# Optimization experiments

Hardware: AMD Instinct MI355X
Metric: run time of the kernel (lower is better)

## Reference

```python
import jax, jax.numpy as jnp
import numpy as np

H = 8  # head_num

def setup_inputs() -> dict:
    key = jax.random.key(0)
    k1, k2, k3, k4, k5 = jax.random.split(key, 5)
    n, e = 4096, 128
    x = jax.random.normal(k1, (n, e), dtype=jnp.float32)
    # torch Linear weights stored here as [in, out]; scale ~ 1/sqrt(fan_in)
    w_qkv = jax.random.normal(k2, (e, e * 3 * H), dtype=jnp.float32) * (1.0 / np.sqrt(e))
    b_qkv = jax.random.normal(k3, (e * 3 * H,), dtype=jnp.float32) * 0.01
    w_proj = jax.random.normal(k4, (e * H, e), dtype=jnp.float32) * (1.0 / np.sqrt(e * H))
    b_proj = jax.random.normal(k5, (e,), dtype=jnp.float32) * 0.01
    return {"x": x, "w_qkv": w_qkv, "b_qkv": b_qkv, "w_proj": w_proj, "b_proj": b_proj}

def reference(x, w_qkv, b_qkv, w_proj, b_proj):
    n, e = x.shape
    # packed layout along output dim is (h, d, qkv) per rearrange 'n (h d qkv) -> qkv h n d'
    qkv = (x @ w_qkv + b_qkv).reshape(n, H, e, 3)          # [n, h, d, 3]
    q = jnp.transpose(qkv[..., 0], (1, 0, 2))              # [h, n, d]
    k = jnp.transpose(qkv[..., 1], (1, 0, 2))
    v = jnp.transpose(qkv[..., 2], (1, 0, 2))
    energy = jnp.einsum('hqd,hkd->hqk', q, k)              # [h, n, n]
    scaling = jnp.asarray(e, x.dtype) ** 0.5
    att = jax.nn.softmax(energy, axis=-1) / scaling        # post-softmax scale (as in source)
    out = jnp.einsum('hqk,hkd->hqd', att, v)               # [h, n, d]
    out = jnp.transpose(out, (1, 0, 2)).reshape(n, H * e)  # [n, h*d]
    return out @ w_proj + b_proj
```

## Files before the change

kernel.cpp:

```cpp
#include <hip/hip_runtime.h>
#include <hip/hip_fp16.h>


#define N_TOK 4096
#define DH 128
#define NH 8

#define EXP2F(x) __builtin_amdgcn_exp2f(x)

typedef _Float16 f16;
typedef __attribute__((ext_vector_type(8))) _Float16 f16x8;
typedef __attribute__((ext_vector_type(2))) __fp16 hf2;
typedef __attribute__((ext_vector_type(4))) float f32x4;

#define GLD16(gsrc, ldst) __builtin_amdgcn_global_load_lds( \
    (const __attribute__((address_space(1))) void*)(gsrc), \
    (__attribute__((address_space(3))) void*)(ldst), 16, 0, 0)

__global__ __launch_bounds__(256) void conv_wproj(
    const float* __restrict__ w_proj, f16* __restrict__ wpT)
{
  int t = blockIdx.x * 256 + threadIdx.x;
  int k = t >> 7, col = t & 127;
  wpT[col * 1024 + k] = (f16)w_proj[t];
}

__global__ __launch_bounds__(256) void conv_wqkv(
    const float* __restrict__ w_qkv, const float* __restrict__ b_qkv,
    f16* __restrict__ wqkvT, float* __restrict__ bperm)
{
  int t = blockIdx.x * 256 + threadIdx.x;
  int k = t / 3072;
  int col = t - k * 3072;
  int hh = col / 384;
  int rem = col - hh * 384;
  int d = rem / 3;
  int s = rem - d * 3;
  int colp = s * 1024 + hh * 128 + d;
  float scale = (s == 0) ? 1.4426950408889634f : 1.0f;
  wqkvT[colp * 128 + k] = (f16)(w_qkv[t] * scale);
  if (k == 0) bperm[colp] = b_qkv[col] * scale;
}

__global__ __launch_bounds__(256) void qkv_gemm2(
    const float* __restrict__ x, const f16* __restrict__ wqkvT,
    const float* __restrict__ bperm,
    f16* __restrict__ Qh, f16* __restrict__ Kh, f16* __restrict__ Vt)
{
  const int cb = blockIdx.x;
  const int rb = blockIdx.y;
  const int tid = threadIdx.x;
  const int w = tid >> 6, lane = tid & 63;
  const int l16 = lane & 15, lhi = lane >> 4;
  const int s = cb >> 3, h = cb & 7;

  f16x8 xf[2][4];
#pragma unroll
  for (int m = 0; m < 2; ++m)
#pragma unroll
    for (int kt = 0; kt < 4; ++kt) {
      const float* xp = x + (size_t)(rb * 128 + w * 32 + m * 16 + l16) * 128 + kt * 32 + lhi * 8;
      f32x4 x0 = *(const f32x4*)xp, x1 = *(const f32x4*)(xp + 4);
      f16x8 v;
#pragma unroll
      for (int j = 0; j < 4; ++j) { v[j] = (f16)x0[j]; v[4 + j] = (f16)x1[j]; }
      xf[m][kt] = v;
    }

  f32x4 acc[8][2];
#pragma unroll
  for (int nt = 0; nt < 8; ++nt)
#pragma unroll
    for (int m = 0; m < 2; ++m) acc[nt][m] = (f32x4){0.f, 0.f, 0.f, 0.f};

#pragma unroll
  for (int nt = 0; nt < 8; ++nt)
#pragma unroll
    for (int kt = 0; kt < 4; ++kt) {
      f16x8 wf = *(const f16x8*)(wqkvT + (size_t)(cb * 128 + nt * 16 + l16) * 128 + kt * 32 + lhi * 8);
      acc[nt][0] = __builtin_amdgcn_mfma_f32_16x16x32_f16(wf, xf[0][kt], acc[nt][0], 0, 0, 0);
      acc[nt][1] = __builtin_amdgcn_mfma_f32_16x16x32_f16(wf, xf[1][kt], acc[nt][1], 0, 0, 0);
    }

#pragma unroll
  for (int nt = 0; nt < 8; ++nt) {
    f32x4 bb = *(const f32x4*)(bperm + cb * 128 + nt * 16 + 4 * lhi);
#pragma unroll
    for (int m = 0; m < 2; ++m) acc[nt][m] += bb;
  }

  if (s == 2) {
#pragma unroll
    for (int nt = 0; nt < 8; ++nt)
#pragma unroll
      for (int m = 0; m < 2; ++m)
#pragma unroll
        for (int r = 0; r < 4; ++r)
          Vt[(size_t)(h * 128 + nt * 16 + 4 * lhi + r) * N_TOK + rb * 128 + w * 32 + m * 16 + l16] =
              (f16)acc[nt][m][r];
  } else {
    __shared__ f16 tr[128][136];
#pragma unroll
    for (int nt = 0; nt < 8; ++nt)
#pragma unroll
      for (int m = 0; m < 2; ++m)
#pragma unroll
        for (int r = 0; r < 4; ++r)
          tr[w * 32 + m * 16 + l16][nt * 16 + 4 * lhi + r] = (f16)acc[nt][m][r];
    __syncthreads();
    f16* dst = (s == 0 ? Qh : Kh) + (size_t)(h * N_TOK + rb * 128) * 128;
    int r = tid >> 1, dh = (tid & 1) * 64;
#pragma unroll
    for (int i = 0; i < 8; ++i)
      *(f16x8*)(dst + r * 128 + dh + i * 8) = *(const f16x8*)(&tr[r][dh + i * 8]);
  }
}

__global__ __launch_bounds__(512, 2) void flash_attn(
    const f16* __restrict__ Qh, const f16* __restrict__ Kh,
    const f16* __restrict__ Vt, f16* __restrict__ opart, float* __restrict__ mlpart)
{
  const int bid = blockIdx.x;
  const int h = bid & 7, sp = (bid >> 3) & 1, qb = bid >> 4;
  const int tid = threadIdx.x;
  const int w = tid >> 6, lane = tid & 63;
  const int l16 = lane & 15, lhi = lane >> 4;

  __shared__ __align__(16) char smem[65536];

  f16x8 qf[2][4];
#pragma unroll
  for (int m = 0; m < 2; ++m)
#pragma unroll
    for (int kt = 0; kt < 4; ++kt)
      qf[m][kt] = *(const f16x8*)(Qh +
          (size_t)(h * N_TOK + qb * 256 + w * 32 + m * 16 + l16) * DH + kt * 32 + lhi * 8);

  int koff[4][4], voff[2][8];
#pragma unroll
  for (int nt = 0; nt < 4; ++nt) {
    int row = 32 * (nt >> 1) + 8 * (l16 >> 2) + 4 * (nt & 1) + (l16 & 3);
    int fk = (row & 3) | ((row & 8) >> 1);
#pragma unroll
    for (int kt = 0; kt < 4; ++kt)
      koff[nt][kt] = row * 256 + ((kt * 4 + lhi) ^ fk) * 16;
  }
#pragma unroll
  for (int ks = 0; ks < 2; ++ks)
#pragma unroll
    for (int dt = 0; dt < 8; ++dt) {
      int rowv = dt * 16 + l16;
      voff[ks][dt] = rowv * 128 + (((ks * 4 + lhi) ^ (rowv & 7))) * 16;
    }

  f32x4 o[2][8];
#pragma unroll
  for (int m = 0; m < 2; ++m)
#pragma unroll
    for (int dt = 0; dt < 8; ++dt) o[m][dt] = (f32x4){0.f, 0.f, 0.f, 0.f};
  float mrun[2] = {-3e38f, -3e38f}, lrun[2] = {0.f, 0.f};

  const f16* Kgh = Kh + (size_t)h * N_TOK * DH;
  const f16* Vgh = Vt + (size_t)h * DH * N_TOK;

  auto stage = [&](int buf, int kb) {
    char* kd = smem + buf * 16384;
    char* vd = smem + 32768 + buf * 16384;
#pragma unroll
    for (int c2 = 0; c2 < 2; ++c2) {
      int c = w * 2 + c2;
      {
        int row = c * 4 + (lane >> 4);
        int fk = (row & 3) | ((row & 8) >> 1);
        const f16* src = Kgh + (size_t)(kb * 64 + row) * DH + ((lane & 15) ^ fk) * 8;
        GLD16(src, kd + c * 1024);
      }
      {
        int row = c * 8 + (lane >> 3);
        const f16* src = Vgh + (size_t)row * N_TOK + kb * 64 + ((lane & 7) ^ (row & 7)) * 8;
        GLD16(src, vd + c * 1024);
      }
    }
  };

  const int kb0 = sp * 32;
  stage(0, kb0);
  __syncthreads();
  int buf = 0;
  for (int kb = kb0; kb < kb0 + 32; ++kb) {
    if (kb < kb0 + 31) stage(buf ^ 1, kb + 1);
    const char* kd = smem + buf * 16384;
    const char* vd = smem + 32768 + buf * 16384;

    f32x4 sv[2][4];
    __builtin_amdgcn_s_setprio(1);
#pragma unroll
    for (int nt = 0; nt < 4; ++nt) {
      f32x4 a0 = {0.f, 0.f, 0.f, 0.f}, a1 = {0.f, 0.f, 0.f, 0.f};
#pragma unroll
      for (int kt = 0; kt < 4; ++kt) {
        f16x8 kf = *(const f16x8*)(kd + koff[nt][kt]);
        a0 = __builtin_amdgcn_mfma_f32_16x16x32_f16(kf, qf[0][kt], a0, 0, 0, 0);
        a1 = __builtin_amdgcn_mfma_f32_16x16x32_f16(kf, qf[1][kt], a1, 0, 0, 0);
      }
      sv[0][nt] = a0; sv[1][nt] = a1;
    }
    __builtin_amdgcn_s_setprio(0);

    f16x8 pf[2][2];
#pragma unroll
    for (int m = 0; m < 2; ++m) {
      f32x4 mv;
#pragma unroll
      for (int r = 0; r < 4; ++r)
        mv[r] = fmaxf(fmaxf(sv[m][0][r], sv[m][1][r]), fmaxf(sv[m][2][r], sv[m][3][r]));
      float pmax = fmaxf(fmaxf(mv[0], mv[1]), fmaxf(mv[2], mv[3]));
      if (!__all(pmax - mrun[m] <= 8.f)) {
        float rm = fmaxf(pmax, __shfl_xor(pmax, 16));
        rm = fmaxf(rm, __shfl_xor(rm, 32));
        float mnew = fmaxf(mrun[m], rm);
        float sc = EXP2F(mrun[m] - mnew);
        lrun[m] *= sc;
#pragma unroll
        for (int dt = 0; dt < 8; ++dt) o[m][dt] *= sc;
        mrun[m] = mnew;
      }
      float mr = mrun[m];
      f32x4 ps = {0.f, 0.f, 0.f, 0.f};
#pragma unroll
      for (int nt = 0; nt < 4; ++nt)
#pragma unroll
        for (int r = 0; r < 4; ++r) {
          float p = EXP2F(sv[m][nt][r] - mr);
          sv[m][nt][r] = p;
          ps[r] += p;
        }
      lrun[m] += (ps[0] + ps[1]) + (ps[2] + ps[3]);
#pragma unroll
      for (int ks = 0; ks < 2; ++ks) {
        union { f16x8 v; hf2 hh[4]; } u;
        u.hh[0] = __builtin_amdgcn_cvt_pkrtz(sv[m][2 * ks][0], sv[m][2 * ks][1]);
        u.hh[1] = __builtin_amdgcn_cvt_pkrtz(sv[m][2 * ks][2], sv[m][2 * ks][3]);
        u.hh[2] = __builtin_amdgcn_cvt_pkrtz(sv[m][2 * ks + 1][0], sv[m][2 * ks + 1][1]);
        u.hh[3] = __builtin_amdgcn_cvt_pkrtz(sv[m][2 * ks + 1][2], sv[m][2 * ks + 1][3]);
        pf[m][ks] = u.v;
      }
    }

    __builtin_amdgcn_s_setprio(1);
#pragma unroll
    for (int ks = 0; ks < 2; ++ks)
#pragma unroll
      for (int dt = 0; dt < 8; ++dt) {
        f16x8 vf = *(const f16x8*)(vd + voff[ks][dt]);
        o[0][dt] = __builtin_amdgcn_mfma_f32_16x16x32_f16(vf, pf[0][ks], o[0][dt], 0, 0, 0);
        o[1][dt] = __builtin_amdgcn_mfma_f32_16x16x32_f16(vf, pf[1][ks], o[1][dt], 0, 0, 0);
      }
    __builtin_amdgcn_s_setprio(0);

    __syncthreads();
    buf ^= 1;
  }

  f16* ob = opart + ((size_t)((sp * 8 + h) * 16 + qb)) * 32768;
  float* mlb = mlpart + ((size_t)((sp * 8 + h) * 16 + qb)) * 512;
#pragma unroll
  for (int m = 0; m < 2; ++m) {
    float lr = lrun[m];
    lr += __shfl_xor(lr, 16);
    lr += __shfl_xor(lr, 32);
    float rl = 1.0f / lr;
#pragma unroll
    for (int dt = 0; dt < 8; ++dt)
#pragma unroll
      for (int r = 0; r < 4; ++r)
        ob[(dt * 16 + 4 * lhi + r) * 256 + w * 32 + m * 16 + l16] = (f16)(o[m][dt][r] * rl);
    if (lhi == 0) {
      mlb[w * 32 + m * 16 + l16] = mrun[m];
      mlb[256 + w * 32 + m * 16 + l16] = lr;
    }
  }
}

__global__ __launch_bounds__(256) void proj_combine(
    const f16* __restrict__ opart, const float* __restrict__ mlpart,
    const f16* __restrict__ wpT, const float* __restrict__ b_proj,
    float* __restrict__ out)
{
  const int tid = threadIdx.x;
  const int w = tid >> 6;
  const int lane = tid & 63;
  const int l16 = lane & 15, lhi = lane >> 4;
  const int rb = blockIdx.x * 16;
  const int qb = rb >> 8;
  const int nl0 = rb & 255;

  __shared__ f16 A[16][1032];
  __shared__ float wl[8][16][3];
  __shared__ float red[4][16][128];

  const float isc = 0.08838834764831845f;
  if (tid < 128) {
    int hh = tid >> 4, n = tid & 15;
    const float* ml0 = mlpart + ((size_t)((0 + hh) * 16 + qb)) * 512 + nl0 + n;
    const float* ml1 = mlpart + ((size_t)((8 + hh) * 16 + qb)) * 512 + nl0 + n;
    float m0 = ml0[0], l0 = ml0[256], m1 = ml1[0], l1 = ml1[256];
    float mt = fmaxf(m0, m1);
    float n0 = EXP2F(m0 - mt) * l0, n1 = EXP2F(m1 - mt) * l1;
    wl[hh][n][0] = n0; wl[hh][n][1] = n1;
    wl[hh][n][2] = isc / (n0 + n1);
  }
  __syncthreads();

  {
    int d = tid >> 1, nn = (tid & 1) * 8;
#pragma unroll
    for (int hh = 0; hh < 8; ++hh) {
      const f16* O0 = opart + ((size_t)((0 + hh) * 16 + qb)) * 32768 + d * 256 + nl0 + nn;
      const f16* O1 = opart + ((size_t)((8 + hh) * 16 + qb)) * 32768 + d * 256 + nl0 + nn;
      f16x8 a0 = *(const f16x8*)O0, a1 = *(const f16x8*)O1;
#pragma unroll
      for (int j = 0; j < 8; ++j) {
        int n = nn + j;
        float v = ((float)a0[j] * wl[hh][n][0] + (float)a1[j] * wl[hh][n][1]) * wl[hh][n][2];
        A[n][hh * 128 + d] = (f16)v;
      }
    }
  }
  __syncthreads();

  f32x4 o[8];
#pragma unroll
  for (int dt = 0; dt < 8; ++dt) o[dt] = (f32x4){0.f, 0.f, 0.f, 0.f};

#pragma unroll
  for (int kb = 0; kb < 8; ++kb) {
    int k0 = w * 256 + kb * 32 + lhi * 8;
    f16x8 a = *(const f16x8*)(&A[l16][k0]);
#pragma unroll
    for (int dt = 0; dt < 8; ++dt) {
      f16x8 b = *(const f16x8*)(wpT + (size_t)(dt * 16 + l16) * 1024 + k0);
      o[dt] = __builtin_amdgcn_mfma_f32_16x16x32_f16(a, b, o[dt], 0, 0, 0);
    }
  }

#pragma unroll
  for (int dt = 0; dt < 8; ++dt)
#pragma unroll
    for (int r = 0; r < 4; ++r)
      red[w][lhi * 4 + r][dt * 16 + l16] = o[dt][r];
  __syncthreads();
#pragma unroll
  for (int i = 0; i < 8; ++i) {
    int idx = tid + 256 * i;
    int row = idx >> 7, col = idx & 127;
    float v = red[0][row][col] + red[1][row][col] + red[2][row][col]
            + red[3][row][col] + b_proj[col];
    out[(size_t)(rb + row) * 128 + col] = v;
  }
}

extern "C" void kernel_launch(void* const* d_in, const int* in_sizes, int n_in,
                              void* d_out, int out_size, void* d_ws, size_t ws_size,
                              hipStream_t stream) {
  const float* x      = (const float*)d_in[0];
  const float* w_qkv  = (const float*)d_in[1];
  const float* b_qkv  = (const float*)d_in[2];
  const float* w_proj = (const float*)d_in[3];
  const float* b_proj = (const float*)d_in[4];
  float* out = (float*)d_out;

  char* ws = (char*)d_ws;
  const size_t MB = 1024 * 1024;
  f16*   Qh     = (f16*)(ws);
  f16*   Kh     = (f16*)(ws + 8 * MB);
  f16*   Vt     = (f16*)(ws + 16 * MB);
  f16*   opart  = (f16*)(ws + 24 * MB);
  float* mlpart = (float*)(ws + 40 * MB);
  f16*   wpT    = (f16*)(ws + 40 * MB + 512 * 1024);
  f16*   wqkvT  = (f16*)(ws + 40 * MB + 768 * 1024);
  float* bperm  = (float*)(ws + 41 * MB + 512 * 1024);

  hipLaunchKernelGGL(conv_wproj, dim3(512), dim3(256), 0, stream, w_proj, wpT);
  hipLaunchKernelGGL(conv_wqkv, dim3(1536), dim3(256), 0, stream, w_qkv, b_qkv, wqkvT, bperm);
  hipLaunchKernelGGL(qkv_gemm2, dim3(24, 32), dim3(256), 0, stream,
                     x, wqkvT, bperm, Qh, Kh, Vt);
  hipLaunchKernelGGL(flash_attn, dim3(256), dim3(512), 0, stream,
                     Qh, Kh, Vt, opart, mlpart);
  hipLaunchKernelGGL(proj_combine, dim3(256), dim3(256), 0, stream,
                     opart, mlpart, wpT, b_proj, out);
}
```

Before: 134.3 us.

## Merge weight conversion kernels and relax flash-attn loop barriers with vmcnt waits

Combines the two weight-conversion kernels into a single launch to save one kernel launch. In the flash attention loop, the full __syncthreads is replaced by an explicit s_waitcnt vmcnt(4) plus a raw s_barrier, so the next tile's global-to-LDS loads stay in flight while the current tile is consumed. The end-of-iteration barrier no longer drains memory counters. This relies on the in-order completion of the global_load_lds ops and on the exact per-thread count of 4 loads; if either assumption is wrong, LDS reads could race.

```diff
diff --git a/kernel.cpp b/kernel.cpp
--- a/kernel.cpp
+++ b/kernel.cpp
@@ -17,29 +17,28 @@
     (const __attribute__((address_space(1))) void*)(gsrc), \
     (__attribute__((address_space(3))) void*)(ldst), 16, 0, 0)
 
-__global__ __launch_bounds__(256) void conv_wproj(
-    const float* __restrict__ w_proj, f16* __restrict__ wpT)
+__global__ __launch_bounds__(256) void conv_weights(
+    const float* __restrict__ w_proj, const float* __restrict__ w_qkv,
+    const float* __restrict__ b_qkv,
+    f16* __restrict__ wpT, f16* __restrict__ wqkvT, float* __restrict__ bperm)
 {
   int t = blockIdx.x * 256 + threadIdx.x;
-  int k = t >> 7, col = t & 127;
-  wpT[col * 1024 + k] = (f16)w_proj[t];
-}
-
-__global__ __launch_bounds__(256) void conv_wqkv(
-    const float* __restrict__ w_qkv, const float* __restrict__ b_qkv,
-    f16* __restrict__ wqkvT, float* __restrict__ bperm)
-{
-  int t = blockIdx.x * 256 + threadIdx.x;
-  int k = t / 3072;
-  int col = t - k * 3072;
-  int hh = col / 384;
-  int rem = col - hh * 384;
-  int d = rem / 3;
-  int s = rem - d * 3;
-  int colp = s * 1024 + hh * 128 + d;
-  float scale = (s == 0) ? 1.4426950408889634f : 1.0f;
-  wqkvT[colp * 128 + k] = (f16)(w_qkv[t] * scale);
-  if (k == 0) bperm[colp] = b_qkv[col] * scale;
+  if (t < 131072) {
+    int k = t >> 7, col = t & 127;
+    wpT[col * 1024 + k] = (f16)w_proj[t];
+  } else {
+    t -= 131072;
+    int k = t / 3072;
+    int col = t - k * 3072;
+    int hh = col / 384;
+    int rem = col - hh * 384;
+    int d = rem / 3;
+    int s = rem - d * 3;
+    int colp = s * 1024 + hh * 128 + d;
+    float scale = (s == 0) ? 1.4426950408889634f : 1.0f;
+    wqkvT[colp * 128 + k] = (f16)(w_qkv[t] * scale);
+    if (k == 0) bperm[colp] = b_qkv[col] * scale;
+  }
 }
 
 __global__ __launch_bounds__(256) void qkv_gemm2(
@@ -185,10 +184,21 @@
 
   const int kb0 = sp * 32;
   stage(0, kb0);
-  __syncthreads();
+  asm volatile("s_waitcnt vmcnt(0)" ::: "memory");
+  __builtin_amdgcn_sched_barrier(0);
+  __builtin_amdgcn_s_barrier();
+
   int buf = 0;
   for (int kb = kb0; kb < kb0 + 32; ++kb) {
-    if (kb < kb0 + 31) stage(buf ^ 1, kb + 1);
+    if (kb < kb0 + 31) {
+      stage(buf ^ 1, kb + 1);
+      asm volatile("s_waitcnt vmcnt(4)" ::: "memory");
+    } else {
+      asm volatile("s_waitcnt vmcnt(0)" ::: "memory");
+    }
+    __builtin_amdgcn_sched_barrier(0);
+    __builtin_amdgcn_s_barrier();
+
     const char* kd = smem + buf * 16384;
     const char* vd = smem + 32768 + buf * 16384;
 
@@ -258,7 +268,7 @@
       }
     __builtin_amdgcn_s_setprio(0);
 
-    __syncthreads();
+    __builtin_amdgcn_s_barrier();
     buf ^= 1;
   }
 
@@ -381,8 +391,8 @@
   f16*   wqkvT  = (f16*)(ws + 40 * MB + 768 * 1024);
   float* bperm  = (float*)(ws + 41 * MB + 512 * 1024);
 
-  hipLaunchKernelGGL(conv_wproj, dim3(512), dim3(256), 0, stream, w_proj, wpT);
-  hipLaunchKernelGGL(conv_wqkv, dim3(1536), dim3(256), 0, stream, w_qkv, b_qkv, wqkvT, bperm);
+  hipLaunchKernelGGL(conv_weights, dim3(2048), dim3(256), 0, stream,
+                     w_proj, w_qkv, b_qkv, wpT, wqkvT, bperm);
   hipLaunchKernelGGL(qkv_gemm2, dim3(24, 32), dim3(256), 0, stream,
                      x, wqkvT, bperm, Qh, Kh, Vt);
   hipLaunchKernelGGL(flash_attn, dim3(256), dim3(512), 0, stream,
```

New measurement: 137.1 us. +2.1%, slower.
